# Kernel tuning notes

Measured on AMD Instinct MI355X. Metric: run time of the kernel, lower is better.

## Reference

```python
import jax, jax.numpy as jnp
import numpy as np

H_GRID, W_GRID = 32, 32
KH, KW = 7, 11
NUM_HEADS = 8


def local_window_mask(H, W, kh, kw):
    # Token (h,w) may attend to (h',w') iff |h-h'|<=kh//2 and |w-w'|<=kw//2
    # (equivalent to the padded/cropped construction in the torch module).
    hh = jnp.arange(H)
    ww = jnp.arange(W)
    ok_h = jnp.abs(hh[:, None] - hh[None, :]) <= kh // 2  # [H,H]
    ok_w = jnp.abs(ww[:, None] - ww[None, :]) <= kw // 2  # [W,W]
    ok = ok_h[:, None, :, None] & ok_w[None, :, None, :]  # [H,W,H,W]
    ok = ok.reshape(H * W, H * W)
    return jnp.where(ok, 0.0, -jnp.inf)[None, None]  # [1,1,N,N]


def setup_inputs() -> dict:
    key = jax.random.key(0)
    k1, k2, k3, k4, k5 = jax.random.split(key, 5)
    B, N, E = 8, H_GRID * W_GRID, 256
    return {
        "x": jax.random.normal(k1, (B, N, E), dtype=jnp.float32),
        "qkv_w": jax.random.normal(k2, (3 * E, E), dtype=jnp.float32) * 0.02,
        "qkv_b": jax.random.normal(k3, (3 * E,), dtype=jnp.float32) * 0.02,
        "proj_w": jax.random.normal(k4, (E, E), dtype=jnp.float32) * 0.02,
        "proj_b": jax.random.normal(k5, (E,), dtype=jnp.float32) * 0.02,
    }


def reference(x, qkv_w, qkv_b, proj_w, proj_b):
    B, N, E = x.shape
    dh = E // NUM_HEADS
    scale = E ** (-0.5)  # note: embed_dim scaling, as in the original module
    qkv = x @ qkv_w.T + qkv_b                       # [B,N,3E]
    qkv = qkv.reshape(B, N, 3, NUM_HEADS, dh).transpose(2, 0, 3, 1, 4)
    q, k, v = qkv[0] * scale, qkv[1], qkv[2]        # [B,H,N,dh]
    attn = jnp.einsum('bhnd,bhmd->bhnm', q, k)      # [B,H,N,N]
    attn = attn + local_window_mask(H_GRID, W_GRID, KH, KW)
    attn = jax.nn.softmax(attn, axis=-1)
    out = jnp.einsum('bhnm,bhmd->bhnd', attn, v)    # [B,H,N,dh]
    out = out.transpose(0, 2, 1, 3).reshape(B, N, E)
    return out @ proj_w.T + proj_b
```

## Files before the change

### kernel.cpp

```cpp
#include <hip/hip_runtime.h>
#include <math.h>

constexpr int Bb = 8;
constexpr int Ns = 1024;
constexpr int Es = 256;
constexpr int NH = 8;
constexpr int DH = 32;
constexpr int Mrows = Bb * Ns;

typedef __bf16 bf16x8 __attribute__((ext_vector_type(8)));
typedef float  f32x4  __attribute__((ext_vector_type(4)));

__device__ __forceinline__ unsigned short f2bf(float f) {
    union { float f; unsigned u; } c; c.f = f;
    unsigned r = (c.u + 0x7FFFu + ((c.u >> 16) & 1u)) >> 16;
    return (unsigned short)r;
}

constexpr int NX = Mrows * Es;
constexpr int NQ = 3 * Es * Es;
constexpr int NP = Es * Es;

__global__ __launch_bounds__(256)
void cast_bf16(const float* __restrict__ x, const float* __restrict__ wq,
               const float* __restrict__ wp, unsigned short* __restrict__ xb,
               unsigned short* __restrict__ wqb, unsigned short* __restrict__ wpb)
{
    int i = (blockIdx.x * 256 + threadIdx.x) * 4;
    const float* src; unsigned short* dst;
    if (i < NX)            { src = x  + i;            dst = xb  + i; }
    else if (i < NX + NQ)  { src = wq + (i - NX);     dst = wqb + (i - NX); }
    else                   { src = wp + (i - NX - NQ); dst = wpb + (i - NX - NQ); }
    float4 f = *(const float4*)src;
    ushort4 u;
    u.x = f2bf(f.x); u.y = f2bf(f.y); u.z = f2bf(f.z); u.w = f2bf(f.w);
    *(ushort4*)dst = u;
}

template<int MODE>
__global__ __launch_bounds__(256)
void gemm_mfma(const unsigned short* __restrict__ A, const unsigned short* __restrict__ W,
               const float* __restrict__ bias,
               float* __restrict__ o0, float* __restrict__ o1, float* __restrict__ o2)
{
    __shared__ unsigned short As[64 * 32];
    __shared__ unsigned short Ws[64 * 32];

    const int t = threadIdx.x;
    const int m0 = blockIdx.x * 64;
    const int j0 = blockIdx.y * 64;

    const int srow = t >> 2;
    const int scol = (t & 3) * 8;

    const int lane = t & 63;
    const int wave = t >> 6;
    const int wm = (wave & 1) * 32;
    const int wn = (wave >> 1) * 32;
    const int fm = lane & 15;
    const int fq = lane >> 4;

    f32x4 acc[2][2];
    #pragma unroll
    for (int i = 0; i < 2; i++)
        #pragma unroll
        for (int j = 0; j < 2; j++)
            acc[i][j] = (f32x4){0.f, 0.f, 0.f, 0.f};

    for (int k0 = 0; k0 < Es; k0 += 32) {
        const uint4 av = *(const uint4*)(A + (size_t)(m0 + srow) * Es + k0 + scol);
        const uint4 wv = *(const uint4*)(W + (size_t)(j0 + srow) * Es + k0 + scol);
        __syncthreads();
        *(uint4*)&As[srow * 32 + scol] = av;
        *(uint4*)&Ws[srow * 32 + scol] = wv;
        __syncthreads();
        bf16x8 a0 = *(const bf16x8*)&As[(wm +      fm) * 32 + fq * 8];
        bf16x8 a1 = *(const bf16x8*)&As[(wm + 16 + fm) * 32 + fq * 8];
        bf16x8 b0 = *(const bf16x8*)&Ws[(wn +      fm) * 32 + fq * 8];
        bf16x8 b1 = *(const bf16x8*)&Ws[(wn + 16 + fm) * 32 + fq * 8];
        acc[0][0] = __builtin_amdgcn_mfma_f32_16x16x32_bf16(a0, b0, acc[0][0], 0, 0, 0);
        acc[0][1] = __builtin_amdgcn_mfma_f32_16x16x32_bf16(a0, b1, acc[0][1], 0, 0, 0);
        acc[1][0] = __builtin_amdgcn_mfma_f32_16x16x32_bf16(a1, b0, acc[1][0], 0, 0, 0);
        acc[1][1] = __builtin_amdgcn_mfma_f32_16x16x32_bf16(a1, b1, acc[1][1], 0, 0, 0);
    }

    #pragma unroll
    for (int mt = 0; mt < 2; mt++) {
        #pragma unroll
        for (int nt = 0; nt < 2; nt++) {
            #pragma unroll
            for (int r = 0; r < 4; r++) {
                int row = m0 + wm + mt * 16 + fq * 4 + r;
                int col = j0 + wn + nt * 16 + fm;
                float val = acc[mt][nt][r] + bias[col];
                if (MODE == 0) {
                    int part = col >> 8;
                    int head = (col >> 5) & 7;
                    int d = col & 31;
                    int b = row >> 10;
                    int n = row & 1023;
                    size_t idx = (((size_t)(b * NH + head)) * Ns + n) * DH + d;
                    if (part == 0)      o0[idx] = val * 0.0625f;
                    else if (part == 1) o1[idx] = val;
                    else                o2[idx] = val;
                } else {
                    o0[(size_t)row * Es + col] = val;
                }
            }
        }
    }
}

#define KVP 36
#define SCP 84

__global__ __launch_bounds__(256)
void attn_win2(const float* __restrict__ q, const float* __restrict__ k,
               const float* __restrict__ v, unsigned short* __restrict__ out)
{
    __shared__ float Qs[32 * KVP];
    __shared__ float Ks[7 * 32 * KVP];
    __shared__ float Vs[7 * 32 * KVP];
    __shared__ float Sc[32 * SCP];

    const int blk = blockIdx.x;
    const int hq  = blk & 31;
    const int bh  = blk >> 5;
    const int t   = threadIdx.x;

    const int sr   = t >> 3;
    const int scol = (t & 7) << 2;

    {
        const float4 qv = *(const float4*)(q + ((size_t)bh * Ns + hq * 32 + sr) * DH + scol);
        *(float4*)&Qs[sr * KVP + scol] = qv;
    }
    #pragma unroll
    for (int r = 0; r < 7; r++) {
        int hh = hq - 3 + r;
        if (hh >= 0 && hh < 32) {
            const float4 kv = *(const float4*)(k + ((size_t)bh * Ns + hh * 32 + sr) * DH + scol);
            const float4 vv = *(const float4*)(v + ((size_t)bh * Ns + hh * 32 + sr) * DH + scol);
            *(float4*)&Ks[(r * 32 + sr) * KVP + scol] = kv;
            *(float4*)&Vs[(r * 32 + sr) * KVP + scol] = vv;
        } else {
            *(float4*)&Vs[(r * 32 + sr) * KVP + scol] = make_float4(0.f, 0.f, 0.f, 0.f);
        }
    }
    __syncthreads();

    const int wq    = t >> 3;
    const int lane8 = t & 7;

    float4 qr[8];
    {
        const float* qrow = &Qs[wq * KVP];
        #pragma unroll
        for (int i = 0; i < 8; i++) qr[i] = *(const float4*)(qrow + i * 4);
    }

    float smax = -INFINITY;
    for (unsigned s = lane8; s < 77u; s += 8u) {
        unsigned dr = s / 11u, dc = s % 11u;
        int hh = hq - 3 + (int)dr;
        int ww = wq - 5 + (int)dc;
        float sc = -INFINITY;
        if (hh >= 0 && hh < 32 && ww >= 0 && ww < 32) {
            const float* krow = &Ks[((int)dr * 32 + ww) * KVP];
            float acc = 0.f;
            #pragma unroll
            for (int i = 0; i < 8; i++) {
                float4 kv = *(const float4*)(krow + i * 4);
                acc = fmaf(qr[i].x, kv.x, acc); acc = fmaf(qr[i].y, kv.y, acc);
                acc = fmaf(qr[i].z, kv.z, acc); acc = fmaf(qr[i].w, kv.w, acc);
            }
            sc = acc;
        }
        Sc[wq * SCP + s] = sc;
        smax = fmaxf(smax, sc);
    }
    #pragma unroll
    for (int m = 1; m < 8; m <<= 1) smax = fmaxf(smax, __shfl_xor(smax, m));

    float lsum = 0.f;
    for (unsigned s = lane8; s < 77u; s += 8u) {
        float p = __expf(Sc[wq * SCP + s] - smax);
        Sc[wq * SCP + s] = p;
        lsum += p;
    }
    #pragma unroll
    for (int m = 1; m < 8; m <<= 1) lsum += __shfl_xor(lsum, m);
    const float inv = 1.f / lsum;

    const int d0 = lane8 << 2;
    float4 acc = make_float4(0.f, 0.f, 0.f, 0.f);
    int sidx = 0;
    #pragma unroll
    for (int dr = 0; dr < 7; dr++) {
        #pragma unroll
        for (int dc = 0; dc < 11; dc++, sidx++) {
            float p = Sc[wq * SCP + sidx];
            int ww = wq - 5 + dc;
            int wwc = ww < 0 ? 0 : (ww > 31 ? 31 : ww);
            float4 vv = *(const float4*)&Vs[(dr * 32 + wwc) * KVP + d0];
            acc.x = fmaf(p, vv.x, acc.x);
            acc.y = fmaf(p, vv.y, acc.y);
            acc.z = fmaf(p, vv.z, acc.z);
            acc.w = fmaf(p, vv.w, acc.w);
        }
    }
    const int b = bh >> 3, h = bh & 7;
    unsigned short* obase = out + ((size_t)(b * Ns + hq * 32 + wq)) * Es + h * DH + d0;
    ushort4 o;
    o.x = f2bf(acc.x * inv); o.y = f2bf(acc.y * inv);
    o.z = f2bf(acc.z * inv); o.w = f2bf(acc.w * inv);
    *(ushort4*)obase = o;
}

extern "C" void kernel_launch(void* const* d_in, const int* in_sizes, int n_in,
                              void* d_out, int out_size, void* d_ws, size_t ws_size,
                              hipStream_t stream) {
    const float* x      = (const float*)d_in[0];
    const float* qkv_w  = (const float*)d_in[1];
    const float* qkv_b  = (const float*)d_in[2];
    const float* proj_w = (const float*)d_in[3];
    const float* proj_b = (const float*)d_in[4];
    float* out = (float*)d_out;

    float* qs = (float*)d_ws;
    float* ks = qs + NX;
    float* vs = ks + NX;
    unsigned short* xb  = (unsigned short*)(vs + NX);
    unsigned short* wqb = xb + NX;
    unsigned short* wpb = wqb + NQ;
    unsigned short* aob = wpb + NP;

    dim3 blk(256);

    cast_bf16<<<dim3((NX + NQ + NP) / 4 / 256), blk, 0, stream>>>(x, qkv_w, proj_w, xb, wqb, wpb);

    dim3 g_qkv(Mrows / 64, (3 * Es) / 64);
    gemm_mfma<0><<<g_qkv, blk, 0, stream>>>(xb, wqb, qkv_b, qs, ks, vs);

    dim3 g_att(Bb * NH * 32);
    attn_win2<<<g_att, blk, 0, stream>>>(qs, ks, vs, aob);

    dim3 g_prj(Mrows / 64, Es / 64);
    gemm_mfma<1><<<g_prj, blk, 0, stream>>>(aob, wpb, proj_b, out, nullptr, nullptr);
}
```

Before: 121.8 us.

## Move windowed attention to bf16 MFMA with bf16 Q/K/transposed-V intermediates

Rewrites the attention kernel to compute Q·K scores and P·V with 16x16x32 bf16 MFMA over a contiguous 224-key band (7 grid rows), applying the window mask during softmax. The QKV GEMM epilogue now writes Q, K and a transposed V in bf16, which halves the intermediate traffic and feeds MFMA B-fragments directly. The GEMM K-tile is doubled to 64 with padded LDS rows. The cost is extra wasted MFMA work on masked keys and bf16 rounding of the probabilities.

```diff
diff --git a/kernel.cpp b/kernel.cpp
--- a/kernel.cpp
+++ b/kernel.cpp
@@ -8,18 +8,23 @@
 constexpr int DH = 32;
 constexpr int Mrows = Bb * Ns;
 
+constexpr int NX = Mrows * Es;
+constexpr int NQ = 3 * Es * Es;
+constexpr int NP = Es * Es;
+
 typedef __bf16 bf16x8 __attribute__((ext_vector_type(8)));
 typedef float  f32x4  __attribute__((ext_vector_type(4)));
+union U4B8 { uint4 u; bf16x8 b; };
 
 __device__ __forceinline__ unsigned short f2bf(float f) {
     union { float f; unsigned u; } c; c.f = f;
     unsigned r = (c.u + 0x7FFFu + ((c.u >> 16) & 1u)) >> 16;
     return (unsigned short)r;
 }
-
-constexpr int NX = Mrows * Es;
-constexpr int NQ = 3 * Es * Es;
-constexpr int NP = Es * Es;
+__device__ __forceinline__ float bf2f(unsigned short h) {
+    union { unsigned u; float f; } c; c.u = ((unsigned)h) << 16;
+    return c.f;
+}
 
 __global__ __launch_bounds__(256)
 void cast_bf16(const float* __restrict__ x, const float* __restrict__ wq,
@@ -28,8 +33,8 @@
 {
     int i = (blockIdx.x * 256 + threadIdx.x) * 4;
     const float* src; unsigned short* dst;
-    if (i < NX)            { src = x  + i;            dst = xb  + i; }
-    else if (i < NX + NQ)  { src = wq + (i - NX);     dst = wqb + (i - NX); }
+    if (i < NX)            { src = x  + i;             dst = xb  + i; }
+    else if (i < NX + NQ)  { src = wq + (i - NX);      dst = wqb + (i - NX); }
     else                   { src = wp + (i - NX - NQ); dst = wpb + (i - NX - NQ); }
     float4 f = *(const float4*)src;
     ushort4 u;
@@ -37,21 +42,24 @@
     *(ushort4*)dst = u;
 }
 
+#define GLD 72
+
 template<int MODE>
 __global__ __launch_bounds__(256)
 void gemm_mfma(const unsigned short* __restrict__ A, const unsigned short* __restrict__ W,
                const float* __restrict__ bias,
-               float* __restrict__ o0, float* __restrict__ o1, float* __restrict__ o2)
+               unsigned short* __restrict__ qo, unsigned short* __restrict__ ko,
+               unsigned short* __restrict__ vto, float* __restrict__ fo)
 {
-    __shared__ unsigned short As[64 * 32];
-    __shared__ unsigned short Ws[64 * 32];
+    __shared__ unsigned short As[64 * GLD];
+    __shared__ unsigned short Ws[64 * GLD];
 
     const int t = threadIdx.x;
     const int m0 = blockIdx.x * 64;
     const int j0 = blockIdx.y * 64;
 
     const int srow = t >> 2;
-    const int scol = (t & 3) * 8;
+    const int scol = (t & 3) * 16;
 
     const int lane = t & 63;
     const int wave = t >> 6;
@@ -67,21 +75,29 @@
         for (int j = 0; j < 2; j++)
             acc[i][j] = (f32x4){0.f, 0.f, 0.f, 0.f};
 
-    for (int k0 = 0; k0 < Es; k0 += 32) {
-        const uint4 av = *(const uint4*)(A + (size_t)(m0 + srow) * Es + k0 + scol);
-        const uint4 wv = *(const uint4*)(W + (size_t)(j0 + srow) * Es + k0 + scol);
+    for (int k0 = 0; k0 < Es; k0 += 64) {
+        const uint4 a0 = *(const uint4*)(A + (size_t)(m0 + srow) * Es + k0 + scol);
+        const uint4 a1 = *(const uint4*)(A + (size_t)(m0 + srow) * Es + k0 + scol + 8);
+        const uint4 w0 = *(const uint4*)(W + (size_t)(j0 + srow) * Es + k0 + scol);
+        const uint4 w1 = *(const uint4*)(W + (size_t)(j0 + srow) * Es + k0 + scol + 8);
         __syncthreads();
-        *(uint4*)&As[srow * 32 + scol] = av;
-        *(uint4*)&Ws[srow * 32 + scol] = wv;
+        *(uint4*)&As[srow * GLD + scol] = a0;
+        *(uint4*)&As[srow * GLD + scol + 8] = a1;
+        *(uint4*)&Ws[srow * GLD + scol] = w0;
+        *(uint4*)&Ws[srow * GLD + scol + 8] = w1;
         __syncthreads();
-        bf16x8 a0 = *(const bf16x8*)&As[(wm +      fm) * 32 + fq * 8];
-        bf16x8 a1 = *(const bf16x8*)&As[(wm + 16 + fm) * 32 + fq * 8];
-        bf16x8 b0 = *(const bf16x8*)&Ws[(wn +      fm) * 32 + fq * 8];
-        bf16x8 b1 = *(const bf16x8*)&Ws[(wn + 16 + fm) * 32 + fq * 8];
-        acc[0][0] = __builtin_amdgcn_mfma_f32_16x16x32_bf16(a0, b0, acc[0][0], 0, 0, 0);
-        acc[0][1] = __builtin_amdgcn_mfma_f32_16x16x32_bf16(a0, b1, acc[0][1], 0, 0, 0);
-        acc[1][0] = __builtin_amdgcn_mfma_f32_16x16x32_bf16(a1, b0, acc[1][0], 0, 0, 0);
-        acc[1][1] = __builtin_amdgcn_mfma_f32_16x16x32_bf16(a1, b1, acc[1][1], 0, 0, 0);
+        #pragma unroll
+        for (int ks = 0; ks < 64; ks += 32) {
+            U4B8 af0, af1, bf0, bf1;
+            af0.u = *(const uint4*)&As[(wm +      fm) * GLD + ks + fq * 8];
+            af1.u = *(const uint4*)&As[(wm + 16 + fm) * GLD + ks + fq * 8];
+            bf0.u = *(const uint4*)&Ws[(wn +      fm) * GLD + ks + fq * 8];
+            bf1.u = *(const uint4*)&Ws[(wn + 16 + fm) * GLD + ks + fq * 8];
+            acc[0][0] = __builtin_amdgcn_mfma_f32_16x16x32_bf16(af0.b, bf0.b, acc[0][0], 0, 0, 0);
+            acc[0][1] = __builtin_amdgcn_mfma_f32_16x16x32_bf16(af0.b, bf1.b, acc[0][1], 0, 0, 0);
+            acc[1][0] = __builtin_amdgcn_mfma_f32_16x16x32_bf16(af1.b, bf0.b, acc[1][0], 0, 0, 0);
+            acc[1][1] = __builtin_amdgcn_mfma_f32_16x16x32_bf16(af1.b, bf1.b, acc[1][1], 0, 0, 0);
+        }
     }
 
     #pragma unroll
@@ -99,122 +115,116 @@
                     int d = col & 31;
                     int b = row >> 10;
                     int n = row & 1023;
-                    size_t idx = (((size_t)(b * NH + head)) * Ns + n) * DH + d;
-                    if (part == 0)      o0[idx] = val * 0.0625f;
-                    else if (part == 1) o1[idx] = val;
-                    else                o2[idx] = val;
+                    int bh = b * NH + head;
+                    if (part == 0)
+                        qo[((size_t)bh * Ns + n) * DH + d] = f2bf(val * 0.0625f);
+                    else if (part == 1)
+                        ko[((size_t)bh * Ns + n) * DH + d] = f2bf(val);
+                    else
+                        vto[((size_t)bh * DH + d) * Ns + n] = f2bf(val);
                 } else {
-                    o0[(size_t)row * Es + col] = val;
+                    fo[(size_t)row * Es + col] = val;
                 }
             }
         }
     }
 }
 
-#define KVP 36
-#define SCP 84
+#define SST 228
+#define PST 232
 
 __global__ __launch_bounds__(256)
-void attn_win2(const float* __restrict__ q, const float* __restrict__ k,
-               const float* __restrict__ v, unsigned short* __restrict__ out)
+void attn_mfma(const unsigned short* __restrict__ qb, const unsigned short* __restrict__ kb,
+               const unsigned short* __restrict__ vtb, unsigned short* __restrict__ aob)
 {
-    __shared__ float Qs[32 * KVP];
-    __shared__ float Ks[7 * 32 * KVP];
-    __shared__ float Vs[7 * 32 * KVP];
-    __shared__ float Sc[32 * SCP];
+    __shared__ float S[32 * SST];
+    __shared__ unsigned short Pb[32 * PST];
+    __shared__ float Linv[32];
 
     const int blk = blockIdx.x;
     const int hq  = blk & 31;
     const int bh  = blk >> 5;
     const int t   = threadIdx.x;
-
-    const int sr   = t >> 3;
-    const int scol = (t & 7) << 2;
-
-    {
-        const float4 qv = *(const float4*)(q + ((size_t)bh * Ns + hq * 32 + sr) * DH + scol);
-        *(float4*)&Qs[sr * KVP + scol] = qv;
-    }
-    #pragma unroll
-    for (int r = 0; r < 7; r++) {
-        int hh = hq - 3 + r;
-        if (hh >= 0 && hh < 32) {
-            const float4 kv = *(const float4*)(k + ((size_t)bh * Ns + hh * 32 + sr) * DH + scol);
-            const float4 vv = *(const float4*)(v + ((size_t)bh * Ns + hh * 32 + sr) * DH + scol);
-            *(float4*)&Ks[(r * 32 + sr) * KVP + scol] = kv;
-            *(float4*)&Vs[(r * 32 + sr) * KVP + scol] = vv;
-        } else {
-            *(float4*)&Vs[(r * 32 + sr) * KVP + scol] = make_float4(0.f, 0.f, 0.f, 0.f);
-        }
+    const int lane = t & 63;
+    const int w    = t >> 6;
+    const int fm = lane & 15;
+    const int fq = lane >> 4;
+
+    int n0c = (hq - 3) * 32;
+    n0c = n0c < 0 ? 0 : (n0c > Ns - 224 ? Ns - 224 : n0c);
+
+    const int qbase = (w & 1) * 16;
+    const int sel   = w >> 1;
+    const int dbase = (w >> 1) * 16;
+
+    const unsigned short* vrow = vtb + ((size_t)bh * DH + dbase + fm) * Ns;
+    uint4 vpre[7];
+    #pragma unroll
+    for (int i = 0; i < 7; i++)
+        vpre[i] = *(const uint4*)(vrow + n0c + i * 32 + fq * 8);
+
+    U4B8 qa;
+    qa.u = *(const uint4*)(qb + ((size_t)bh * Ns + hq * 32 + qbase + fm) * DH + fq * 8);
+
+    #pragma unroll
+    for (int i = 0; i < 7; i++) {
+        int kt = sel + 2 * i;
+        U4B8 kf;
+        kf.u = *(const uint4*)(kb + ((size_t)bh * Ns + n0c + kt * 16 + fm) * DH + fq * 8);
+        f32x4 s = __builtin_amdgcn_mfma_f32_16x16x32_bf16(qa.b, kf.b, (f32x4){0.f,0.f,0.f,0.f}, 0, 0, 0);
+        #pragma unroll
+        for (int r = 0; r < 4; r++)
+            S[(qbase + fq * 4 + r) * SST + kt * 16 + fm] = s[r];
     }
     __syncthreads();
 
-    const int wq    = t >> 3;
-    const int lane8 = t & 7;
-
-    float4 qr[8];
-    {
-        const float* qrow = &Qs[wq * KVP];
-        #pragma unroll
-        for (int i = 0; i < 8; i++) qr[i] = *(const float4*)(qrow + i * 4);
-    }
-
+    const int sq = t >> 3;
+    const int l8 = t & 7;
+    float sv[28];
     float smax = -INFINITY;
-    for (unsigned s = lane8; s < 77u; s += 8u) {
-        unsigned dr = s / 11u, dc = s % 11u;
-        int hh = hq - 3 + (int)dr;
-        int ww = wq - 5 + (int)dc;
-        float sc = -INFINITY;
-        if (hh >= 0 && hh < 32 && ww >= 0 && ww < 32) {
-            const float* krow = &Ks[((int)dr * 32 + ww) * KVP];
-            float acc = 0.f;
-            #pragma unroll
-            for (int i = 0; i < 8; i++) {
-                float4 kv = *(const float4*)(krow + i * 4);
-                acc = fmaf(qr[i].x, kv.x, acc); acc = fmaf(qr[i].y, kv.y, acc);
-                acc = fmaf(qr[i].z, kv.z, acc); acc = fmaf(qr[i].w, kv.w, acc);
-            }
-            sc = acc;
-        }
-        Sc[wq * SCP + s] = sc;
-        smax = fmaxf(smax, sc);
+    #pragma unroll
+    for (int i = 0; i < 28; i++) {
+        int j = l8 + 8 * i;
+        int g = n0c + j;
+        int gh = g >> 5, gw = g & 31;
+        int dh_ = gh - hq, dw_ = gw - sq;
+        bool ok = (dh_ >= -3) && (dh_ <= 3) && (dw_ >= -5) && (dw_ <= 5);
+        float x = ok ? S[sq * SST + j] : -INFINITY;
+        sv[i] = x;
+        smax = fmaxf(smax, x);
     }
     #pragma unroll
     for (int m = 1; m < 8; m <<= 1) smax = fmaxf(smax, __shfl_xor(smax, m));
 
     float lsum = 0.f;
-    for (unsigned s = lane8; s < 77u; s += 8u) {
-        float p = __expf(Sc[wq * SCP + s] - smax);
-        Sc[wq * SCP + s] = p;
-        lsum += p;
+    #pragma unroll
+    for (int i = 0; i < 28; i++) {
+        float p = __expf(sv[i] - smax);
+        unsigned short pu = f2bf(p);
+        Pb[sq * PST + l8 + 8 * i] = pu;
+        lsum += bf2f(pu);
     }
     #pragma unroll
     for (int m = 1; m < 8; m <<= 1) lsum += __shfl_xor(lsum, m);
-    const float inv = 1.f / lsum;
-
-    const int d0 = lane8 << 2;
-    float4 acc = make_float4(0.f, 0.f, 0.f, 0.f);
-    int sidx = 0;
-    #pragma unroll
-    for (int dr = 0; dr < 7; dr++) {
-        #pragma unroll
-        for (int dc = 0; dc < 11; dc++, sidx++) {
-            float p = Sc[wq * SCP + sidx];
-            int ww = wq - 5 + dc;
-            int wwc = ww < 0 ? 0 : (ww > 31 ? 31 : ww);
-            float4 vv = *(const float4*)&Vs[(dr * 32 + wwc) * KVP + d0];
-            acc.x = fmaf(p, vv.x, acc.x);
-            acc.y = fmaf(p, vv.y, acc.y);
-            acc.z = fmaf(p, vv.z, acc.z);
-            acc.w = fmaf(p, vv.w, acc.w);
-        }
-    }
+    if (l8 == 0) Linv[sq] = 1.f / lsum;
+    __syncthreads();
+
+    f32x4 acc = (f32x4){0.f, 0.f, 0.f, 0.f};
+    #pragma unroll
+    for (int i = 0; i < 7; i++) {
+        U4B8 pa, vb;
+        pa.u = *(const uint4*)&Pb[(qbase + fm) * PST + i * 32 + fq * 8];
+        vb.u = vpre[i];
+        acc = __builtin_amdgcn_mfma_f32_16x16x32_bf16(pa.b, vb.b, acc, 0, 0, 0);
+    }
+
     const int b = bh >> 3, h = bh & 7;
-    unsigned short* obase = out + ((size_t)(b * Ns + hq * 32 + wq)) * Es + h * DH + d0;
-    ushort4 o;
-    o.x = f2bf(acc.x * inv); o.y = f2bf(acc.y * inv);
-    o.z = f2bf(acc.z * inv); o.w = f2bf(acc.w * inv);
-    *(ushort4*)obase = o;
+    #pragma unroll
+    for (int r = 0; r < 4; r++) {
+        int qq = qbase + fq * 4 + r;
+        float o = acc[r] * Linv[qq];
+        aob[((size_t)(b * Ns) + hq * 32 + qq) * Es + h * DH + dbase + fm] = f2bf(o);
+    }
 }
 
 extern "C" void kernel_launch(void* const* d_in, const int* in_sizes, int n_in,
@@ -227,24 +237,24 @@
     const float* proj_b = (const float*)d_in[4];
     float* out = (float*)d_out;
 
-    float* qs = (float*)d_ws;
-    float* ks = qs + NX;
-    float* vs = ks + NX;
-    unsigned short* xb  = (unsigned short*)(vs + NX);
+    unsigned short* xb  = (unsigned short*)d_ws;
     unsigned short* wqb = xb + NX;
     unsigned short* wpb = wqb + NQ;
-    unsigned short* aob = wpb + NP;
+    unsigned short* qb  = wpb + NP;
+    unsigned short* kb  = qb + NX;
+    unsigned short* vtb = kb + NX;
+    unsigned short* aob = vtb + NX;
 
     dim3 blk(256);
 
     cast_bf16<<<dim3((NX + NQ + NP) / 4 / 256), blk, 0, stream>>>(x, qkv_w, proj_w, xb, wqb, wpb);
 
     dim3 g_qkv(Mrows / 64, (3 * Es) / 64);
-    gemm_mfma<0><<<g_qkv, blk, 0, stream>>>(xb, wqb, qkv_b, qs, ks, vs);
+    gemm_mfma<0><<<g_qkv, blk, 0, stream>>>(xb, wqb, qkv_b, qb, kb, vtb, nullptr);
 
     dim3 g_att(Bb * NH * 32);
-    attn_win2<<<g_att, blk, 0, stream>>>(qs, ks, vs, aob);
+    attn_mfma<<<g_att, blk, 0, stream>>>(qb, kb, vtb, aob);
 
     dim3 g_prj(Mrows / 64, Es / 64);
-    gemm_mfma<1><<<g_prj, blk, 0, stream>>>(aob, wpb, proj_b, out, nullptr, nullptr);
-}
+    gemm_mfma<1><<<g_prj, blk, 0, stream>>>(aob, wpb, proj_b, nullptr, nullptr, nullptr, out);
+}
```

Result: faster. 103.9 us (-14.7%).
